# Optimization experiments

Measured on AMD Instinct MI355X. Metric: run time of the kernel, lower is better.

## Reference

```python
import jax, jax.numpy as jnp
import numpy as np

D_MODEL = 1024
NUM_HEADS = 16
D_K = D_MODEL // NUM_HEADS


def setup_inputs() -> dict:
    key = jax.random.key(0)
    ks = jax.random.split(key, 12)
    B, S = 4, 2048
    scale = 1.0 / np.sqrt(D_MODEL)
    inp = {
        "query": jax.random.normal(ks[0], (B, S, D_MODEL), dtype=jnp.float32),
        "key": jax.random.normal(ks[1], (B, S, D_MODEL), dtype=jnp.float32),
        "value": jax.random.normal(ks[2], (B, S, D_MODEL), dtype=jnp.float32),
        "Wq": jax.random.normal(ks[3], (D_MODEL, D_MODEL), dtype=jnp.float32) * scale,
        "bq": jnp.zeros((D_MODEL,), dtype=jnp.float32),
        "Wk": jax.random.normal(ks[4], (D_MODEL, D_MODEL), dtype=jnp.float32) * scale,
        "bk": jnp.zeros((D_MODEL,), dtype=jnp.float32),
        "Wv": jax.random.normal(ks[5], (D_MODEL, D_MODEL), dtype=jnp.float32) * scale,
        "bv": jnp.zeros((D_MODEL,), dtype=jnp.float32),
        "Wo": jax.random.normal(ks[6], (D_MODEL, D_MODEL), dtype=jnp.float32) * scale,
        "bo": jnp.zeros((D_MODEL,), dtype=jnp.float32),
    }
    return inp


def reference(query, key, value, Wq, bq, Wk, bk, Wv, bv, Wo, bo):
    B, S, _ = query.shape
    # project and split heads: [B, S, D] -> [B, H, S, d_k]
    def split_heads(x):
        return x.reshape(B, -1, NUM_HEADS, D_K).transpose(0, 2, 1, 3)

    q = split_heads(query @ Wq + bq)
    k = split_heads(key @ Wk + bk)
    v = split_heads(value @ Wv + bv)

    # scores: [B, H, Sq, Sk]
    scores = jnp.einsum("bhqd,bhkd->bhqk", q, k) / jnp.sqrt(jnp.float32(D_K))
    p_attn = jax.nn.softmax(scores, axis=-1)
    out = jnp.einsum("bhqk,bhkd->bhqd", p_attn, v)  # [B, H, Sq, d_k]

    out = out.transpose(0, 2, 1, 3).reshape(B, -1, NUM_HEADS * D_K)
    return out @ Wo + bo
```

## Files before the change

### kernel.cpp

```cpp
#include <hip/hip_runtime.h>
#include <hip/hip_bf16.h>

#define D_MODEL 1024
#define SEQ     2048
#define BATCH   4
#define HEADS   16
#define DKK     64
#define MTOT    (BATCH*SEQ)

typedef __attribute__((ext_vector_type(8)))  __bf16 bf16x8;
typedef __attribute__((ext_vector_type(4)))  float  f32x4;
typedef __attribute__((ext_vector_type(16))) float  f32x16;
typedef unsigned short u16;
typedef __attribute__((address_space(1))) const unsigned GU;
typedef __attribute__((address_space(3))) unsigned LU;

__device__ __forceinline__ u16 f2bf(float f) {
    unsigned u = __builtin_bit_cast(unsigned, f);
    u += 0x7FFFu + ((u >> 16) & 1u);
    return (u16)(u >> 16);
}

__device__ __forceinline__ unsigned pk2(float a, float b) {
    u16 x = __builtin_bit_cast(u16, (__bf16)a);
    u16 y = __builtin_bit_cast(u16, (__bf16)b);
    return (unsigned)x | ((unsigned)y << 16);
}

__device__ __forceinline__ float exp2_hw(float x) {
    return __builtin_amdgcn_exp2f(x);
}

__global__ void wtrans4_kernel(const float* __restrict__ W0, const float* __restrict__ W1,
                               const float* __restrict__ W2, const float* __restrict__ W3,
                               u16* __restrict__ T0, u16* __restrict__ T1,
                               u16* __restrict__ T2, u16* __restrict__ T3) {
    const float* W = (blockIdx.z == 0) ? W0 : (blockIdx.z == 1) ? W1 : (blockIdx.z == 2) ? W2 : W3;
    u16* Wt = (blockIdx.z == 0) ? T0 : (blockIdx.z == 1) ? T1 : (blockIdx.z == 2) ? T2 : T3;
    __shared__ float t[32][33];
    int bx = blockIdx.x * 32, by = blockIdx.y * 32;
    int x = threadIdx.x, y0 = threadIdx.y;
    for (int y = y0; y < 32; y += 8)
        t[y][x] = W[(size_t)(by + y) * D_MODEL + bx + x];
    __syncthreads();
    for (int y = y0; y < 32; y += 8)
        Wt[(size_t)(bx + y) * D_MODEL + by + x] = f2bf(t[x][y]);
}

__global__ __launch_bounds__(512) void gemm_qkv(
        const float* __restrict__ A0, const float* __restrict__ A1, const float* __restrict__ A2,
        const u16* __restrict__ B0, const u16* __restrict__ B1, const u16* __restrict__ B2,
        const float* __restrict__ bi0, const float* __restrict__ bi1, const float* __restrict__ bi2,
        u16* __restrict__ o0, u16* __restrict__ o1, u16* __restrict__ o2, float qscale)
{
    __shared__ __align__(16) char smem[3][16384];

    const int lin = blockIdx.x;
    const int xcd = lin & 7, slot = lin >> 3;
    const int cpx = gridDim.x >> 3;
    const int work = xcd * cpx + slot;
    const int xb = work & 7;
    const int yz = work >> 3;
    const int z = yz >> 6, yb = yz & 63;
    const int m0 = yb * 128, n0 = xb * 128;

    const float* A = (z == 0) ? A0 : (z == 1) ? A1 : A2;
    const u16* Bt = (z == 0) ? B0 : (z == 1) ? B1 : B2;
    const float* bias = (z == 0) ? bi0 : (z == 1) ? bi1 : bi2;
    u16* outb = (z == 0) ? o0 : (z == 1) ? o1 : o2;
    const float scale = (z == 0) ? qscale : 1.0f;

    const int tid = threadIdx.x;
    const int w = tid >> 6, lane = tid & 63;
    const int l15 = lane & 15, lg = lane >> 4;
    const int wr = w >> 2, wc = w & 3;

    f32x4 acc[4][2];
#pragma unroll
    for (int i = 0; i < 4; i++)
#pragma unroll
        for (int j = 0; j < 2; j++) acc[i][j] = (f32x4){0.f, 0.f, 0.f, 0.f};

    const float* Ab = A + (size_t)(m0 + (tid >> 2)) * D_MODEL + (tid & 3) * 8;
    float4 aw, ax;

    auto loadA = [&](int k0) {
        const float* p0 = Ab + k0;
        aw = *reinterpret_cast<const float4*>(p0);
        ax = *reinterpret_cast<const float4*>(p0 + 4);
    };
    auto cvtWriteA = [&](int buf) {
        u16* Al = (u16*)(smem[buf]);
        union { u16 e[8]; bf16x8 v; } u0;
        u0.e[0] = f2bf(aw.x); u0.e[1] = f2bf(aw.y); u0.e[2] = f2bf(aw.z); u0.e[3] = f2bf(aw.w);
        u0.e[4] = f2bf(ax.x); u0.e[5] = f2bf(ax.y); u0.e[6] = f2bf(ax.z); u0.e[7] = f2bf(ax.w);
        *reinterpret_cast<bf16x8*>(Al + tid * 8) = u0.v;
    };
    auto gldsB = [&](int buf, int k0) {
        u16* Bl = (u16*)(smem[buf] + 8192);
        __builtin_amdgcn_global_load_lds(
            (GU*)(Bt + (size_t)(n0 + (tid >> 2)) * D_MODEL + k0 + (tid & 3) * 8),
            (LU*)(Bl + tid * 8), 16, 0, 0);
    };

    auto compute = [&](int buf) {
        const u16* Al = (const u16*)(smem[buf]);
        const u16* Bl = (const u16*)(smem[buf] + 8192);
        bf16x8 af[4], bfr[2];
#pragma unroll
        for (int m = 0; m < 4; m++)
            af[m] = *reinterpret_cast<const bf16x8*>(&Al[(wr * 64 + m * 16 + l15) * 32 + lg * 8]);
#pragma unroll
        for (int n = 0; n < 2; n++)
            bfr[n] = *reinterpret_cast<const bf16x8*>(&Bl[(wc * 32 + n * 16 + l15) * 32 + lg * 8]);
        __builtin_amdgcn_s_setprio(1);
#pragma unroll
        for (int m = 0; m < 4; m++)
#pragma unroll
            for (int n = 0; n < 2; n++)
                acc[m][n] = __builtin_amdgcn_mfma_f32_16x16x32_bf16(af[m], bfr[n], acc[m][n], 0, 0, 0);
        __builtin_amdgcn_s_setprio(0);
    };

    loadA(0);  gldsB(0, 0);
    cvtWriteA(0);
    loadA(32); gldsB(1, 32);
    for (int t = 0; t < 32; ++t) {
        if (t < 31) asm volatile("s_waitcnt vmcnt(3)" ::: "memory");
        else        asm volatile("s_waitcnt vmcnt(0)" ::: "memory");
        asm volatile("s_waitcnt lgkmcnt(0)" ::: "memory");
        __builtin_amdgcn_s_barrier();
        __builtin_amdgcn_sched_barrier(0);
        if (t < 31) cvtWriteA((t + 1) % 3);
        if (t + 2 < 32) { loadA((t + 2) * 32); gldsB((t + 2) % 3, (t + 2) * 32); }
        compute(t % 3);
    }

    if (z == 2) {
        __syncthreads();
        typedef u16 TRow[136];
        TRow* T = reinterpret_cast<TRow*>(smem);
#pragma unroll
        for (int n = 0; n < 2; n++) {
            int colL = wc * 32 + n * 16 + l15;
            float bv = bias[n0 + colL];
#pragma unroll
            for (int m = 0; m < 4; m++) {
                int rowL = wr * 64 + m * 16 + lg * 4;
#pragma unroll
                for (int r = 0; r < 4; r++)
                    T[colL][rowL + r] = f2bf(acc[m][n][r] + bv);
            }
        }
        __syncthreads();
        {
            int col = tid >> 2, q = tid & 3;
            int colG = n0 + col;
            int h = colG >> 6, d = colG & 63;
            int b = m0 >> 11, s0r = (m0 & (SEQ - 1)) + q * 32;
            u16* dst = outb + (((size_t)b * HEADS + h) * DKK + d) * SEQ + s0r;
            const u16* src = &T[col][q * 32];
#pragma unroll
            for (int c = 0; c < 4; c++)
                *reinterpret_cast<bf16x8*>(dst + c * 8) =
                    *reinterpret_cast<const bf16x8*>(src + c * 8);
        }
        return;
    }
#pragma unroll
    for (int n = 0; n < 2; n++) {
        int col = n0 + wc * 32 + n * 16 + l15;
        float bv = bias[col];
        int h = col >> 6, d = col & 63;
#pragma unroll
        for (int m = 0; m < 4; m++) {
            int rowb = m0 + wr * 64 + m * 16 + lg * 4;
            int b = rowb >> 11, s0r = rowb & (SEQ - 1);
#pragma unroll
            for (int r = 0; r < 4; r++)
                outb[(((size_t)b * HEADS + h) * SEQ + s0r + r) * DKK + d] =
                    f2bf((acc[m][n][r] + bv) * scale);
        }
    }
}

__global__ __launch_bounds__(512) void gemm_out(
        const u16* __restrict__ A, const u16* __restrict__ Bt,
        const float* __restrict__ bias, float* __restrict__ outf)
{
    __shared__ __align__(16) char smem[3][16384];

    const int lin = blockIdx.x;
    const int xcd = lin & 7, slot = lin >> 3;
    const int cpx = gridDim.x >> 3;
    const int work = xcd * cpx + slot;
    const int xb = work & 7, yb = work >> 3;
    const int m0 = yb * 128, n0 = xb * 128;

    const int tid = threadIdx.x;
    const int w = tid >> 6, lane = tid & 63;
    const int l15 = lane & 15, lg = lane >> 4;
    const int wr = w >> 2, wc = w & 3;

    f32x4 acc[4][2];
#pragma unroll
    for (int i = 0; i < 4; i++)
#pragma unroll
        for (int j = 0; j < 2; j++) acc[i][j] = (f32x4){0.f, 0.f, 0.f, 0.f};

    auto stage = [&](int buf, int k0) {
        u16* Al = (u16*)(smem[buf]);
        u16* Bl = (u16*)(smem[buf] + 8192);
        int row = tid >> 2, ch = tid & 3;
        __builtin_amdgcn_global_load_lds(
            (GU*)(A + (size_t)(m0 + row) * D_MODEL + k0 + ch * 8),
            (LU*)(Al + tid * 8), 16, 0, 0);
        __builtin_amdgcn_global_load_lds(
            (GU*)(Bt + (size_t)(n0 + row) * D_MODEL + k0 + ch * 8),
            (LU*)(Bl + tid * 8), 16, 0, 0);
    };
    auto compute = [&](int buf) {
        const u16* Al = (const u16*)(smem[buf]);
        const u16* Bl = (const u16*)(smem[buf] + 8192);
        bf16x8 af[4], bfr[2];
#pragma unroll
        for (int m = 0; m < 4; m++)
            af[m] = *reinterpret_cast<const bf16x8*>(&Al[(wr * 64 + m * 16 + l15) * 32 + lg * 8]);
#pragma unroll
        for (int n = 0; n < 2; n++)
            bfr[n] = *reinterpret_cast<const bf16x8*>(&Bl[(wc * 32 + n * 16 + l15) * 32 + lg * 8]);
        __builtin_amdgcn_s_setprio(1);
#pragma unroll
        for (int m = 0; m < 4; m++)
#pragma unroll
            for (int n = 0; n < 2; n++)
                acc[m][n] = __builtin_amdgcn_mfma_f32_16x16x32_bf16(af[m], bfr[n], acc[m][n], 0, 0, 0);
        __builtin_amdgcn_s_setprio(0);
    };

    stage(0, 0);
    stage(1, 32);
    for (int t = 0; t < 32; ++t) {
        if (t < 31) asm volatile("s_waitcnt vmcnt(2)" ::: "memory");
        else        asm volatile("s_waitcnt vmcnt(0)" ::: "memory");
        __builtin_amdgcn_s_barrier();
        __builtin_amdgcn_sched_barrier(0);
        if (t + 2 < 32) stage((t + 2) % 3, (t + 2) * 32);
        compute(t % 3);
    }

#pragma unroll
    for (int n = 0; n < 2; n++) {
        int col = n0 + wc * 32 + n * 16 + l15;
        float bv = bias[col];
#pragma unroll
        for (int m = 0; m < 4; m++) {
            int rowb = m0 + wr * 64 + m * 16 + lg * 4;
#pragma unroll
            for (int r = 0; r < 4; r++)
                outf[(size_t)(rowb + r) * D_MODEL + col] = acc[m][n][r] + bv;
        }
    }
}

__global__ __launch_bounds__(512, 2) void attn9_kernel(
        const u16* __restrict__ Qh, const u16* __restrict__ Kh,
        const u16* __restrict__ VT, u16* __restrict__ ctx)
{
    __shared__ __align__(16) char smem[3][16384];

    const int i = blockIdx.x;
    const int xcd = i & 7, j = i >> 3;
    const int bh = xcd + 8 * (j & 7);
    const int bx = j >> 3;
    const int b = bh >> 4, h = bh & 15;
    const int tid = threadIdx.x, w = tid >> 6, lane = tid & 63;
    const int l31 = lane & 31, hi = lane >> 5;
    const int q0 = bx * 256 + w * 32;

    const u16* Qp = Qh + ((size_t)bh * SEQ + q0 + l31) * DKK + 8 * hi;
    bf16x8 qf[4];
#pragma unroll
    for (int c = 0; c < 4; c++)
        qf[c] = *reinterpret_cast<const bf16x8*>(Qp + 16 * c);

    const char* Kbyte = (const char*)(Kh + (size_t)bh * SEQ * DKK);
    const char* Vbyte = (const char*)(VT + (size_t)bh * DKK * SEQ);

    f32x16 zv;
#pragma unroll
    for (int z = 0; z < 16; z++) zv[z] = 0.f;
    f32x16 oacc0 = zv, oacc1 = zv;
    float lsum = 0.f;

    const int kr = tid >> 3, kc = tid & 7;
    const int ksw = (kc ^ (kr & 7)) * 16;
    const int krp = (kr & 51) | ((kr & 4) << 1) | ((kr & 8) >> 1);

    auto stage = [&](int buf, int kt) {
        char* Kb = smem[buf];
        char* Vb = smem[buf] + 8192;
        __builtin_amdgcn_global_load_lds((GU*)(Kbyte + (size_t)(kt + krp) * 128 + ksw),
                                         (LU*)(Kb + tid * 16), 16, 0, 0);
        __builtin_amdgcn_global_load_lds((GU*)(Vbyte + (size_t)kr * (SEQ * 2) + kt * 2 + ksw),
                                         (LU*)(Vb + tid * 16), 16, 0, 0);
    };

    auto compute = [&](int buf) {
        const char* Kb = smem[buf];
        const char* Vb = smem[buf] + 8192;
        const int xr = (l31 & 7);

        bf16x8 kf[8];
#pragma unroll
        for (int c = 0; c < 4; c++) {
            int sl = ((2 * c + hi) ^ xr) * 16;
            kf[c]     = *reinterpret_cast<const bf16x8*>(Kb + l31 * 128 + sl);
            kf[c + 4] = *reinterpret_cast<const bf16x8*>(Kb + (l31 + 32) * 128 + sl);
        }

        __builtin_amdgcn_s_setprio(1);
        f32x16 s0 = __builtin_amdgcn_mfma_f32_32x32x16_bf16(kf[0], qf[0], zv, 0, 0, 0);
        f32x16 s1 = __builtin_amdgcn_mfma_f32_32x32x16_bf16(kf[4], qf[0], zv, 0, 0, 0);
#pragma unroll
        for (int c = 1; c < 4; c++) {
            s0 = __builtin_amdgcn_mfma_f32_32x32x16_bf16(kf[c],     qf[c], s0, 0, 0, 0);
            s1 = __builtin_amdgcn_mfma_f32_32x32x16_bf16(kf[c + 4], qf[c], s1, 0, 0, 0);
        }
        __builtin_amdgcn_s_setprio(0);

#pragma unroll
        for (int i2 = 0; i2 < 16; i2++) { s0[i2] = exp2_hw(s0[i2]); s1[i2] = exp2_hw(s1[i2]); }
        float a0 = (s0[0] + s0[1]) + (s0[2] + s0[3]);
        float a1 = (s0[4] + s0[5]) + (s0[6] + s0[7]);
        float a2 = (s0[8] + s0[9]) + (s0[10] + s0[11]);
        float a3 = (s0[12] + s0[13]) + (s0[14] + s0[15]);
        float b0 = (s1[0] + s1[1]) + (s1[2] + s1[3]);
        float b1 = (s1[4] + s1[5]) + (s1[6] + s1[7]);
        float b2 = (s1[8] + s1[9]) + (s1[10] + s1[11]);
        float b3 = (s1[12] + s1[13]) + (s1[14] + s1[15]);
        lsum += ((a0 + a1) + (a2 + a3)) + ((b0 + b1) + (b2 + b3));

#pragma unroll
        for (int t = 0; t < 4; t++) {
            const int o = 8 * (t & 1);
            union { unsigned u[4]; bf16x8 v; } pu;
            if (t < 2) {
                pu.u[0] = pk2(s0[o+0], s0[o+1]);
                pu.u[1] = pk2(s0[o+2], s0[o+3]);
                pu.u[2] = pk2(s0[o+4], s0[o+5]);
                pu.u[3] = pk2(s0[o+6], s0[o+7]);
            } else {
                pu.u[0] = pk2(s1[o+0], s1[o+1]);
                pu.u[1] = pk2(s1[o+2], s1[o+3]);
                pu.u[2] = pk2(s1[o+4], s1[o+5]);
                pu.u[3] = pk2(s1[o+6], s1[o+7]);
            }
            bf16x8 pf = pu.v;

            int sl = ((2 * t + hi) ^ xr) * 16;
            bf16x8 vf0 = *reinterpret_cast<const bf16x8*>(Vb + l31 * 128 + sl);
            bf16x8 vf1 = *reinterpret_cast<const bf16x8*>(Vb + (l31 + 32) * 128 + sl);
            __builtin_amdgcn_s_setprio(1);
            oacc0 = __builtin_amdgcn_mfma_f32_32x32x16_bf16(vf0, pf, oacc0, 0, 0, 0);
            oacc1 = __builtin_amdgcn_mfma_f32_32x32x16_bf16(vf1, pf, oacc1, 0, 0, 0);
            __builtin_amdgcn_s_setprio(0);
        }
    };

    stage(0, 0);
    stage(1, 64);
    for (int t = 0; t < 32; ++t) {
        if (t < 31) asm volatile("s_waitcnt vmcnt(2)" ::: "memory");
        else        asm volatile("s_waitcnt vmcnt(0)" ::: "memory");
        __builtin_amdgcn_s_barrier();
        __builtin_amdgcn_sched_barrier(0);
        if (t + 2 < 32) stage((t + 2) % 3, (t + 2) * 64);
        compute(t % 3);
    }
    __syncthreads();

    lsum += __shfl_xor(lsum, 32, 64);
    float inv = 1.0f / lsum;

    typedef u16 OtArr[32][72];
    OtArr* Ot = reinterpret_cast<OtArr*>(smem);
#pragma unroll
    for (int r = 0; r < 16; r++) {
        int d0 = (r & 3) + 8 * (r >> 2) + 4 * hi;
        Ot[w][l31][d0]      = f2bf(oacc0[r] * inv);
        Ot[w][l31][d0 + 32] = f2bf(oacc1[r] * inv);
    }
    __syncthreads();
#pragma unroll
    for (int it = 0; it < 4; it++) {
        int r = (lane >> 3) + 8 * it, ch = lane & 7;
        bf16x8 v = *reinterpret_cast<const bf16x8*>(&Ot[w][r][ch * 8]);
        *reinterpret_cast<bf16x8*>(ctx + ((size_t)b * SEQ + q0 + r) * D_MODEL + h * DKK + ch * 8) = v;
    }
}

extern "C" void kernel_launch(void* const* d_in, const int* in_sizes, int n_in,
                              void* d_out, int out_size, void* d_ws, size_t ws_size,
                              hipStream_t stream)
{
    (void)in_sizes; (void)n_in; (void)out_size; (void)ws_size;

    const float* query = (const float*)d_in[0];
    const float* key   = (const float*)d_in[1];
    const float* value = (const float*)d_in[2];
    const float* Wq    = (const float*)d_in[3];
    const float* bq    = (const float*)d_in[4];
    const float* Wk    = (const float*)d_in[5];
    const float* bk    = (const float*)d_in[6];
    const float* Wv    = (const float*)d_in[7];
    const float* bv    = (const float*)d_in[8];
    const float* Wo    = (const float*)d_in[9];
    const float* bo    = (const float*)d_in[10];
    float* out = (float*)d_out;

    char* ws = (char*)d_ws;
    const size_t MB = 1024ull * 1024ull;
    u16* Wtq = (u16*)(ws + 48 * MB);
    u16* Wtk = (u16*)(ws + 50 * MB);
    u16* Wtv = (u16*)(ws + 52 * MB);
    u16* Wto = (u16*)(ws + 54 * MB);
    u16* Qhp = (u16*)(ws + 56 * MB);
    u16* Khp = (u16*)(ws + 72 * MB);
    u16* VT  = (u16*)(ws + 88 * MB);
    u16* ctx = (u16*)(ws + 104 * MB);

    dim3 wg(32, 32, 4), wb(32, 8);
    wtrans4_kernel<<<wg, wb, 0, stream>>>(Wq, Wk, Wv, Wo, Wtq, Wtk, Wtv, Wto);

    gemm_qkv<<<1536, 512, 0, stream>>>(query, key, value, Wtq, Wtk, Wtv, bq, bk, bv,
                                       Qhp, Khp, VT, 0.125f * 1.44269504f);

    attn9_kernel<<<512, 512, 0, stream>>>(Qhp, Khp, VT, ctx);

    gemm_out<<<512, 512, 0, stream>>>(ctx, Wto, bo, out);
}
```

Measured before the change: 199.7 us.

## Double K-tile to 64 and switch QKV GEMM to a double-buffered pipeline

The QKV projection GEMM now processes a K-slice of 64 per stage instead of 32. Each thread loads two A chunks and issues two direct-to-LDS B loads per stage. The LDS ring changes from three 16KB stages to two 32KB stages, and the main loop is reordered to 16 iterations with adjusted vmcnt waits. This halves the number of barriers and loop iterations and gives more MFMA work per synchronisation, at the cost of more LDS per block, more live registers for the A prefetch, and less prefetch depth.

```diff
diff --git a/kernel.cpp b/kernel.cpp
--- a/kernel.cpp
+++ b/kernel.cpp
@@ -53,7 +53,7 @@
         const float* __restrict__ bi0, const float* __restrict__ bi1, const float* __restrict__ bi2,
         u16* __restrict__ o0, u16* __restrict__ o1, u16* __restrict__ o2, float qscale)
 {
-    __shared__ __align__(16) char smem[3][16384];
+    __shared__ __align__(16) char smem[2][32768];
 
     const int lin = blockIdx.x;
     const int xcd = lin & 7, slot = lin >> 3;
@@ -81,59 +81,77 @@
 #pragma unroll
         for (int j = 0; j < 2; j++) acc[i][j] = (f32x4){0.f, 0.f, 0.f, 0.f};
 
-    const float* Ab = A + (size_t)(m0 + (tid >> 2)) * D_MODEL + (tid & 3) * 8;
-    float4 aw, ax;
+    const int ar1 = tid >> 3,          ac1 = tid & 7;
+    const int ar2 = (tid + 512) >> 3,  ac2 = tid & 7;
+    const float* Ab1 = A + (size_t)(m0 + ar1) * D_MODEL + ac1 * 8;
+    const float* Ab2 = A + (size_t)(m0 + ar2) * D_MODEL + ac2 * 8;
+    float4 aw, ax, ay, az_;
 
     auto loadA = [&](int k0) {
-        const float* p0 = Ab + k0;
-        aw = *reinterpret_cast<const float4*>(p0);
-        ax = *reinterpret_cast<const float4*>(p0 + 4);
+        aw  = *reinterpret_cast<const float4*>(Ab1 + k0);
+        ax  = *reinterpret_cast<const float4*>(Ab1 + k0 + 4);
+        ay  = *reinterpret_cast<const float4*>(Ab2 + k0);
+        az_ = *reinterpret_cast<const float4*>(Ab2 + k0 + 4);
     };
     auto cvtWriteA = [&](int buf) {
         u16* Al = (u16*)(smem[buf]);
-        union { u16 e[8]; bf16x8 v; } u0;
+        union { u16 e[8]; bf16x8 v; } u0, u1;
         u0.e[0] = f2bf(aw.x); u0.e[1] = f2bf(aw.y); u0.e[2] = f2bf(aw.z); u0.e[3] = f2bf(aw.w);
         u0.e[4] = f2bf(ax.x); u0.e[5] = f2bf(ax.y); u0.e[6] = f2bf(ax.z); u0.e[7] = f2bf(ax.w);
+        u1.e[0] = f2bf(ay.x); u1.e[1] = f2bf(ay.y); u1.e[2] = f2bf(ay.z); u1.e[3] = f2bf(ay.w);
+        u1.e[4] = f2bf(az_.x); u1.e[5] = f2bf(az_.y); u1.e[6] = f2bf(az_.z); u1.e[7] = f2bf(az_.w);
         *reinterpret_cast<bf16x8*>(Al + tid * 8) = u0.v;
+        *reinterpret_cast<bf16x8*>(Al + (tid + 512) * 8) = u1.v;
     };
     auto gldsB = [&](int buf, int k0) {
-        u16* Bl = (u16*)(smem[buf] + 8192);
+        u16* Bl = (u16*)(smem[buf] + 16384);
         __builtin_amdgcn_global_load_lds(
-            (GU*)(Bt + (size_t)(n0 + (tid >> 2)) * D_MODEL + k0 + (tid & 3) * 8),
+            (GU*)(Bt + (size_t)(n0 + ar1) * D_MODEL + k0 + ac1 * 8),
             (LU*)(Bl + tid * 8), 16, 0, 0);
+        __builtin_amdgcn_global_load_lds(
+            (GU*)(Bt + (size_t)(n0 + ar2) * D_MODEL + k0 + ac2 * 8),
+            (LU*)(Bl + (tid + 512) * 8), 16, 0, 0);
     };
 
     auto compute = [&](int buf) {
         const u16* Al = (const u16*)(smem[buf]);
-        const u16* Bl = (const u16*)(smem[buf] + 8192);
-        bf16x8 af[4], bfr[2];
-#pragma unroll
-        for (int m = 0; m < 4; m++)
-            af[m] = *reinterpret_cast<const bf16x8*>(&Al[(wr * 64 + m * 16 + l15) * 32 + lg * 8]);
-#pragma unroll
-        for (int n = 0; n < 2; n++)
-            bfr[n] = *reinterpret_cast<const bf16x8*>(&Bl[(wc * 32 + n * 16 + l15) * 32 + lg * 8]);
-        __builtin_amdgcn_s_setprio(1);
-#pragma unroll
-        for (int m = 0; m < 4; m++)
+        const u16* Bl = (const u16*)(smem[buf] + 16384);
+#pragma unroll
+        for (int hh = 0; hh < 2; hh++) {
+            bf16x8 af[4], bfr[2];
+#pragma unroll
+            for (int m = 0; m < 4; m++)
+                af[m] = *reinterpret_cast<const bf16x8*>(
+                    &Al[(wr * 64 + m * 16 + l15) * 64 + hh * 32 + lg * 8]);
 #pragma unroll
             for (int n = 0; n < 2; n++)
-                acc[m][n] = __builtin_amdgcn_mfma_f32_16x16x32_bf16(af[m], bfr[n], acc[m][n], 0, 0, 0);
-        __builtin_amdgcn_s_setprio(0);
+                bfr[n] = *reinterpret_cast<const bf16x8*>(
+                    &Bl[(wc * 32 + n * 16 + l15) * 64 + hh * 32 + lg * 8]);
+            __builtin_amdgcn_s_setprio(1);
+#pragma unroll
+            for (int m = 0; m < 4; m++)
+#pragma unroll
+                for (int n = 0; n < 2; n++)
+                    acc[m][n] = __builtin_amdgcn_mfma_f32_16x16x32_bf16(af[m], bfr[n], acc[m][n], 0, 0, 0);
+            __builtin_amdgcn_s_setprio(0);
+        }
     };
 
     loadA(0);  gldsB(0, 0);
+    __builtin_amdgcn_sched_barrier(0);
     cvtWriteA(0);
-    loadA(32); gldsB(1, 32);
-    for (int t = 0; t < 32; ++t) {
-        if (t < 31) asm volatile("s_waitcnt vmcnt(3)" ::: "memory");
+    loadA(64);
+    for (int t = 0; t < 16; ++t) {
+        if (t < 15) asm volatile("s_waitcnt vmcnt(4)" ::: "memory");
         else        asm volatile("s_waitcnt vmcnt(0)" ::: "memory");
         asm volatile("s_waitcnt lgkmcnt(0)" ::: "memory");
         __builtin_amdgcn_s_barrier();
         __builtin_amdgcn_sched_barrier(0);
-        if (t < 31) cvtWriteA((t + 1) % 3);
-        if (t + 2 < 32) { loadA((t + 2) * 32); gldsB((t + 2) % 3, (t + 2) * 32); }
-        compute(t % 3);
+        if (t + 1 < 16) gldsB((t + 1) & 1, (t + 1) * 64);
+        __builtin_amdgcn_sched_barrier(0);
+        if (t + 1 < 16) cvtWriteA((t + 1) & 1);
+        if (t + 2 < 16) loadA((t + 2) * 64);
+        compute(t & 1);
     }
 
     if (z == 2) {
```

New measurement: 216.1 us. 1.08x slower.
